# Optimization experiments

Hardware: AMD Instinct MI355X
Metric: run time of the kernel (lower is better)

The kernel has to match this reference:

```python
import jax, jax.numpy as jnp
import numpy as np

OUT_GRID = (256, 256)  # output_grid_shape


def setup_inputs() -> dict:
    key = jax.random.key(0)
    k1, k2 = jax.random.split(key)
    N, H, W, C = 16, 256, 256, 32
    x = jax.random.normal(k1, (N, H, W, C), dtype=jnp.float32)
    # loc network: global mean pool -> dense(6); small weights + identity-affine bias
    W_loc = jax.random.normal(k2, (C, 6), dtype=jnp.float32) * 0.01
    b_loc = jnp.array([1.0, 0.0, 0.0, 0.0, 1.0, 0.0], dtype=jnp.float32)
    return {"x": x, "W_loc": W_loc, "b_loc": b_loc}


def _spatial_transform(x, W_loc, b_loc):
    N, H, W, C = x.shape
    Ho, Wo = OUT_GRID
    # loc_network: params (N, 6) -> theta (N, 2, 3)
    params = jnp.mean(x, axis=(1, 2)) @ W_loc + b_loc
    theta = params.reshape(N, 2, 3)
    # grid_transform_fn: affine on [-1,1]-normalized output index grid
    gy = jnp.linspace(-1.0, 1.0, Ho, dtype=jnp.float32)
    gx = jnp.linspace(-1.0, 1.0, Wo, dtype=jnp.float32)
    Gy, Gx = jnp.meshgrid(gy, gx, indexing="ij")
    grid = jnp.stack([Gy.ravel(), Gx.ravel(), jnp.ones(Ho * Wo, jnp.float32)], axis=0)  # (3, Ho*Wo)
    coords = jnp.einsum("npq,qm->npm", theta, grid).reshape(N, 2, Ho, Wo)  # in ~[-1,1]
    # interpolate_bilinear with clip (wrap=False)
    maxes = jnp.array([H - 1, W - 1], dtype=jnp.float32)
    up = (coords + 1.0) * maxes[None, :, None, None] * 0.5  # upscale to pixel coords
    f = jnp.floor(up)
    frac = up - f  # (N, 2, Ho, Wo)
    fi = f.astype(jnp.int32)
    batch = jnp.arange(N)[:, None, None]
    out = jnp.zeros((N, Ho, Wo, C), dtype=x.dtype)
    for by in (0, 1):  # 2^dim corner offsets (bitfield)
        for bx in (0, 1):
            cy = jnp.clip(fi[:, 0] + by, 0, H - 1)
            cx = jnp.clip(fi[:, 1] + bx, 0, W - 1)
            wy = frac[:, 0] if by else 1.0 - frac[:, 0]
            wx = frac[:, 1] if bx else 1.0 - frac[:, 1]
            out = out + x[batch, cy, cx] * (wy * wx)[..., None]
    return out


def reference(x, W_loc, b_loc):
    return _spatial_transform(x, W_loc, b_loc)
```

## Files before the change

### kernel.cpp

```cpp
#include <hip/hip_runtime.h>


#define NIMG 16
#define HDIM 256
#define WDIM 256
#define CH   32
#define HW   (HDIM * WDIM)
#define BPI  64
#define STAGE_PX 384

typedef float f32x4 __attribute__((ext_vector_type(4)));

__global__ __launch_bounds__(256) void st_sum_kernel(
    const float* __restrict__ x, float* __restrict__ partials) {
    const int n   = blockIdx.x >> 6;
    const int blk = blockIdx.x & (BPI - 1);
    const int tid = threadIdx.x;
    const int cg  = tid & 7;
    const int sp  = tid >> 3;

    const float4* xp = (const float4*)(x + (size_t)n * HW * CH);
    float4 a0 = make_float4(0.f, 0.f, 0.f, 0.f);
    float4 a1 = make_float4(0.f, 0.f, 0.f, 0.f);
    float4 a2 = make_float4(0.f, 0.f, 0.f, 0.f);
    float4 a3 = make_float4(0.f, 0.f, 0.f, 0.f);
    int s = blk * 32 + sp;
    #pragma unroll
    for (int it = 0; it < 8; ++it) {
        float4 v0 = xp[(size_t)(s       ) * 8 + cg];
        float4 v1 = xp[(size_t)(s + 2048) * 8 + cg];
        float4 v2 = xp[(size_t)(s + 4096) * 8 + cg];
        float4 v3 = xp[(size_t)(s + 6144) * 8 + cg];
        a0.x += v0.x; a0.y += v0.y; a0.z += v0.z; a0.w += v0.w;
        a1.x += v1.x; a1.y += v1.y; a1.z += v1.z; a1.w += v1.w;
        a2.x += v2.x; a2.y += v2.y; a2.z += v2.z; a2.w += v2.w;
        a3.x += v3.x; a3.y += v3.y; a3.z += v3.z; a3.w += v3.w;
        s += 8192;
    }
    a0.x += a1.x; a0.y += a1.y; a0.z += a1.z; a0.w += a1.w;
    a2.x += a3.x; a2.y += a3.y; a2.z += a3.z; a2.w += a3.w;
    a0.x += a2.x; a0.y += a2.y; a0.z += a2.z; a0.w += a2.w;

    __shared__ float4 red[256];
    red[tid] = a0;
    __syncthreads();
    for (int stride = 16; stride >= 1; stride >>= 1) {
        if (sp < stride) {
            float4 o = red[(sp + stride) * 8 + cg];
            a0.x += o.x; a0.y += o.y; a0.z += o.z; a0.w += o.w;
            red[tid] = a0;
        }
        __syncthreads();
    }
    if (sp == 0) {
        ((float4*)(partials + ((size_t)blk * NIMG + n) * CH))[cg] = a0;
    }
}

__global__ __launch_bounds__(256) void st_interp_kernel(
    const float* __restrict__ x, const float* __restrict__ partials,
    const float* __restrict__ W_loc, const float* __restrict__ b_loc,
    float* __restrict__ out) {
    const int bid = (int)blockIdx.x;
    const int swz = (bid & 7) * 512 + (bid >> 3);
    const int n   = swz >> 8;
    const int r   = swz & 255;
    const int tid = threadIdx.x;

    __shared__ float  red2[8][CH];
    __shared__ float  th_s[8];
    __shared__ float4 stage[STAGE_PX * 8];

    {
        const int c = tid & 31, g = tid >> 5;
        float s = 0.f;
        #pragma unroll
        for (int j = 0; j < 8; ++j)
            s += partials[(size_t)((g * 8 + j) * NIMG + n) * CH + c];
        red2[g][c] = s;
        __syncthreads();
        if (g == 0) {
            float m = 0.f;
            #pragma unroll
            for (int j = 0; j < 8; ++j) m += red2[j][c];
            red2[0][c] = m * (1.0f / (float)HW);
        }
        __syncthreads();
        if (tid < 6) {
            float acc = b_loc[tid];
            for (int c2 = 0; c2 < CH; ++c2)
                acc = fmaf(red2[0][c2], W_loc[c2 * 6 + tid], acc);
            th_s[tid] = acc;
        }
        __syncthreads();
    }
    const float t00 = th_s[0], t01 = th_s[1], t02 = th_s[2];
    const float t10 = th_s[3], t11 = th_s[4], t12 = th_s[5];

    const int ty = r >> 3, tx = r & 7;
    const int row0 = ty * 8, col0 = tx * 32;
    const int p  = tid >> 3;
    const int cg = tid & 7;
    const int wo = col0 + p;

    const float gx  = fmaf((float)wo, 2.0f / 255.0f, -1.0f);
    const float ayx = fmaf(t01, gx, t02);
    const float axx = fmaf(t11, gx, t12);

    const float gyA = fmaf((float)row0,        2.0f / 255.0f, -1.0f);
    const float gyB = fmaf((float)(row0 + 7),  2.0f / 255.0f, -1.0f);
    const float gxA = fmaf((float)col0,        2.0f / 255.0f, -1.0f);
    const float gxB = fmaf((float)(col0 + 31), 2.0f / 255.0f, -1.0f);
    const float uy1 = (fmaf(t00, gyA, fmaf(t01, gxA, t02)) + 1.0f) * 127.5f;
    const float uy2 = (fmaf(t00, gyA, fmaf(t01, gxB, t02)) + 1.0f) * 127.5f;
    const float uy3 = (fmaf(t00, gyB, fmaf(t01, gxA, t02)) + 1.0f) * 127.5f;
    const float uy4 = (fmaf(t00, gyB, fmaf(t01, gxB, t02)) + 1.0f) * 127.5f;
    const float ux1 = (fmaf(t10, gyA, fmaf(t11, gxA, t12)) + 1.0f) * 127.5f;
    const float ux2 = (fmaf(t10, gyA, fmaf(t11, gxB, t12)) + 1.0f) * 127.5f;
    const float ux3 = (fmaf(t10, gyB, fmaf(t11, gxA, t12)) + 1.0f) * 127.5f;
    const float ux4 = (fmaf(t10, gyB, fmaf(t11, gxB, t12)) + 1.0f) * 127.5f;
    const float uymin = fminf(fminf(uy1, uy2), fminf(uy3, uy4));
    const float uymax = fmaxf(fmaxf(uy1, uy2), fmaxf(uy3, uy4));
    const float uxmin = fminf(fminf(ux1, ux2), fminf(ux3, ux4));
    const float uxmax = fmaxf(fmaxf(ux1, ux2), fmaxf(ux3, ux4));
    const int iy_lo = min(max((int)floorf(uymin),     0), HDIM - 1);
    const int iy_hi = min(max((int)floorf(uymax) + 1, 0), HDIM - 1);
    const int ix_lo = min(max((int)floorf(uxmin),     0), WDIM - 1);
    const int ix_hi = min(max((int)floorf(uxmax) + 1, 0), WDIM - 1);
    const int Rr = iy_hi - iy_lo + 1;
    const int Cc = ix_hi - ix_lo + 1;
    const bool finite = (uymin == uymin) && (uymax == uymax) &&
                        (uxmin == uxmin) && (uxmax == uxmax);
    const bool fits = finite && Rr >= 1 && Cc >= 1 && (Rr * Cc) <= STAGE_PX;

    const float4* xp = (const float4*)(x + (size_t)n * HW * CH);
    f32x4* op = (f32x4*)(out + (size_t)n * HW * CH);

    if (fits) {
        const int C8 = Cc * 8;
        for (int rr = 0; rr < Rr; ++rr) {
            const float4* src = xp + ((size_t)((iy_lo + rr) * WDIM + ix_lo)) * 8;
            float4* dst = stage + rr * C8;
            for (int u = tid; u < C8; u += 256) dst[u] = src[u];
        }
        __syncthreads();

        #pragma unroll
        for (int k = 0; k < 8; ++k) {
            const int ho = row0 + k;
            const float gy = fmaf((float)ho, 2.0f / 255.0f, -1.0f);
            const float uy = (fmaf(t00, gy, ayx) + 1.0f) * 127.5f;
            const float ux = (fmaf(t10, gy, axx) + 1.0f) * 127.5f;
            const float fy = floorf(uy), fx = floorf(ux);
            const float ry = uy - fy, rx = ux - fx;
            const int iy0 = min(max((int)fy,     0), HDIM - 1);
            const int iy1 = min(max((int)fy + 1, 0), HDIM - 1);
            const int ix0 = min(max((int)fx,     0), WDIM - 1);
            const int ix1 = min(max((int)fx + 1, 0), WDIM - 1);
            const int ly0 = iy0 - iy_lo, ly1 = iy1 - iy_lo;
            const int lx0 = ix0 - ix_lo, lx1 = ix1 - ix_lo;
            float4 v00 = stage[(ly0 * Cc + lx0) * 8 + cg];
            float4 v01 = stage[(ly0 * Cc + lx1) * 8 + cg];
            float4 v10 = stage[(ly1 * Cc + lx0) * 8 + cg];
            float4 v11 = stage[(ly1 * Cc + lx1) * 8 + cg];
            const float w00 = (1.0f - ry) * (1.0f - rx);
            const float w01 = (1.0f - ry) * rx;
            const float w10 = ry * (1.0f - rx);
            const float w11 = ry * rx;
            f32x4 o;
            o.x = v00.x * w00 + v01.x * w01 + v10.x * w10 + v11.x * w11;
            o.y = v00.y * w00 + v01.y * w01 + v10.y * w10 + v11.y * w11;
            o.z = v00.z * w00 + v01.z * w01 + v10.z * w10 + v11.z * w11;
            o.w = v00.w * w00 + v01.w * w01 + v10.w * w10 + v11.w * w11;
            __builtin_nontemporal_store(o, &op[(size_t)(ho * WDIM + wo) * 8 + cg]);
        }
    } else {
        for (int k = 0; k < 8; ++k) {
            const int ho = row0 + k;
            const float gy = fmaf((float)ho, 2.0f / 255.0f, -1.0f);
            const float uy = (fmaf(t00, gy, ayx) + 1.0f) * 127.5f;
            const float ux = (fmaf(t10, gy, axx) + 1.0f) * 127.5f;
            const float fy = floorf(uy), fx = floorf(ux);
            const float ry = uy - fy, rx = ux - fx;
            const int iy0 = min(max((int)fy,     0), HDIM - 1);
            const int iy1 = min(max((int)fy + 1, 0), HDIM - 1);
            const int ix0 = min(max((int)fx,     0), WDIM - 1);
            const int ix1 = min(max((int)fx + 1, 0), WDIM - 1);
            float4 v00 = xp[(size_t)(iy0 * WDIM + ix0) * 8 + cg];
            float4 v01 = xp[(size_t)(iy0 * WDIM + ix1) * 8 + cg];
            float4 v10 = xp[(size_t)(iy1 * WDIM + ix0) * 8 + cg];
            float4 v11 = xp[(size_t)(iy1 * WDIM + ix1) * 8 + cg];
            const float w00 = (1.0f - ry) * (1.0f - rx);
            const float w01 = (1.0f - ry) * rx;
            const float w10 = ry * (1.0f - rx);
            const float w11 = ry * rx;
            f32x4 o;
            o.x = v00.x * w00 + v01.x * w01 + v10.x * w10 + v11.x * w11;
            o.y = v00.y * w00 + v01.y * w01 + v10.y * w10 + v11.y * w11;
            o.z = v00.z * w00 + v01.z * w01 + v10.z * w10 + v11.z * w11;
            o.w = v00.w * w00 + v01.w * w01 + v10.w * w10 + v11.w * w11;
            __builtin_nontemporal_store(o, &op[(size_t)(ho * WDIM + wo) * 8 + cg]);
        }
    }
}

extern "C" void kernel_launch(void* const* d_in, const int* in_sizes, int n_in,
                              void* d_out, int out_size, void* d_ws, size_t ws_size,
                              hipStream_t stream) {
    const float* x     = (const float*)d_in[0];
    const float* W_loc = (const float*)d_in[1];
    const float* b_loc = (const float*)d_in[2];
    float* out = (float*)d_out;

    float* partials = (float*)d_ws;

    st_sum_kernel<<<NIMG * BPI, 256, 0, stream>>>(x, partials);
    st_interp_kernel<<<NIMG * (HW / 256), 256, 0, stream>>>(
        x, partials, W_loc, b_loc, out);
}
```

Baseline: 75.60 us.

## Speculatively prefetch fixed halo window into registers before theta computation

The interp kernel now issues the global loads for a fixed 10x36-pixel window around the output tile, with a 1-row and 2-column halo, into registers before it reduces partials and computes theta. The tile loads therefore overlap the loc-network latency instead of waiting on it. The values are written to LDS only if the transformed footprint falls inside this fixed window, which near-identity affines should satisfy; otherwise the existing global-gather fallback runs. This costs 12 float4 registers per thread and a possibly wasted load when the window misses, and a fixed stride removes the dynamic Cc indexing.

```diff
diff --git a/kernel.cpp b/kernel.cpp
--- a/kernel.cpp
+++ b/kernel.cpp
@@ -7,7 +7,12 @@
 #define CH   32
 #define HW   (HDIM * WDIM)
 #define BPI  64
-#define STAGE_PX 384
+
+#define R_CAP 10
+#define C_CAP 36
+#define C8    (C_CAP * 8)
+#define STAGE_N (R_CAP * C8)
+#define NLD   12
 
 typedef float f32x4 __attribute__((ext_vector_type(4)));
 
@@ -67,9 +72,28 @@
     const int r   = swz & 255;
     const int tid = threadIdx.x;
 
+    const int ty = r >> 3, tx = r & 7;
+    const int row0 = ty * 8, col0 = tx * 32;
+
     __shared__ float  red2[8][CH];
     __shared__ float  th_s[8];
-    __shared__ float4 stage[STAGE_PX * 8];
+    __shared__ float4 stage[STAGE_N];
+
+    const float4* xp = (const float4*)(x + (size_t)n * HW * CH);
+
+    float4 buf[NLD];
+    #pragma unroll
+    for (int i = 0; i < NLD; ++i) {
+        const int u = tid + i * 256;
+        if (u < STAGE_N) {
+            const int rr  = u / C8;
+            const int m   = u - rr * C8;
+            const int lx  = m >> 3, c2 = m & 7;
+            const int sy  = min(max(row0 - 1 + rr, 0), HDIM - 1);
+            const int sx  = min(max(col0 - 2 + lx, 0), WDIM - 1);
+            buf[i] = xp[(size_t)(sy * WDIM + sx) * 8 + c2];
+        }
+    }
 
     {
         const int c = tid & 31, g = tid >> 5;
@@ -96,16 +120,6 @@
     }
     const float t00 = th_s[0], t01 = th_s[1], t02 = th_s[2];
     const float t10 = th_s[3], t11 = th_s[4], t12 = th_s[5];
-
-    const int ty = r >> 3, tx = r & 7;
-    const int row0 = ty * 8, col0 = tx * 32;
-    const int p  = tid >> 3;
-    const int cg = tid & 7;
-    const int wo = col0 + p;
-
-    const float gx  = fmaf((float)wo, 2.0f / 255.0f, -1.0f);
-    const float ayx = fmaf(t01, gx, t02);
-    const float axx = fmaf(t11, gx, t12);
 
     const float gyA = fmaf((float)row0,        2.0f / 255.0f, -1.0f);
     const float gyB = fmaf((float)(row0 + 7),  2.0f / 255.0f, -1.0f);
@@ -117,34 +131,33 @@
     const float uy4 = (fmaf(t00, gyB, fmaf(t01, gxB, t02)) + 1.0f) * 127.5f;
     const float ux1 = (fmaf(t10, gyA, fmaf(t11, gxA, t12)) + 1.0f) * 127.5f;
     const float ux2 = (fmaf(t10, gyA, fmaf(t11, gxB, t12)) + 1.0f) * 127.5f;
-    const float ux3 = (fmaf(t10, gyB, fmaf(t11, gxA, t12)) + 1.0f) * 127.5f;
-    const float ux4 = (fmaf(t10, gyB, fmaf(t11, gxB, t12)) + 1.0f) * 127.5f;
+    const float ux3 = (fmaf(t10, gyB, fmaf(t11, gxB, t12)) + 1.0f) * 127.5f;
+    const float ux4 = (fmaf(t10, gyB, fmaf(t11, gxA, t12)) + 1.0f) * 127.5f;
     const float uymin = fminf(fminf(uy1, uy2), fminf(uy3, uy4));
     const float uymax = fmaxf(fmaxf(uy1, uy2), fmaxf(uy3, uy4));
     const float uxmin = fminf(fminf(ux1, ux2), fminf(ux3, ux4));
     const float uxmax = fmaxf(fmaxf(ux1, ux2), fmaxf(ux3, ux4));
-    const int iy_lo = min(max((int)floorf(uymin),     0), HDIM - 1);
-    const int iy_hi = min(max((int)floorf(uymax) + 1, 0), HDIM - 1);
-    const int ix_lo = min(max((int)floorf(uxmin),     0), WDIM - 1);
-    const int ix_hi = min(max((int)floorf(uxmax) + 1, 0), WDIM - 1);
-    const int Rr = iy_hi - iy_lo + 1;
-    const int Cc = ix_hi - ix_lo + 1;
-    const bool finite = (uymin == uymin) && (uymax == uymax) &&
-                        (uxmin == uxmin) && (uxmax == uxmax);
-    const bool fits = finite && Rr >= 1 && Cc >= 1 && (Rr * Cc) <= STAGE_PX;
-
-    const float4* xp = (const float4*)(x + (size_t)n * HW * CH);
+    const bool fits = (uymin > (float)row0 - 0.9f) && (uymax < (float)row0 + 7.9f) &&
+                      (uxmin > (float)col0 - 1.9f) && (uxmax < (float)col0 + 32.9f);
+
+    const int p  = tid >> 3;
+    const int cg = tid & 7;
+    const int wo = col0 + p;
+    const float gx  = fmaf((float)wo, 2.0f / 255.0f, -1.0f);
+    const float ayx = fmaf(t01, gx, t02);
+    const float axx = fmaf(t11, gx, t12);
+
     f32x4* op = (f32x4*)(out + (size_t)n * HW * CH);
 
     if (fits) {
-        const int C8 = Cc * 8;
-        for (int rr = 0; rr < Rr; ++rr) {
-            const float4* src = xp + ((size_t)((iy_lo + rr) * WDIM + ix_lo)) * 8;
-            float4* dst = stage + rr * C8;
-            for (int u = tid; u < C8; u += 256) dst[u] = src[u];
-        }
-        __syncthreads();
-
+        #pragma unroll
+        for (int i = 0; i < NLD; ++i) {
+            const int u = tid + i * 256;
+            if (u < STAGE_N) stage[u] = buf[i];
+        }
+        __syncthreads();
+
+        const int iy_lo = row0 - 1, ix_lo = col0 - 2;
         #pragma unroll
         for (int k = 0; k < 8; ++k) {
             const int ho = row0 + k;
@@ -159,10 +172,10 @@
             const int ix1 = min(max((int)fx + 1, 0), WDIM - 1);
             const int ly0 = iy0 - iy_lo, ly1 = iy1 - iy_lo;
             const int lx0 = ix0 - ix_lo, lx1 = ix1 - ix_lo;
-            float4 v00 = stage[(ly0 * Cc + lx0) * 8 + cg];
-            float4 v01 = stage[(ly0 * Cc + lx1) * 8 + cg];
-            float4 v10 = stage[(ly1 * Cc + lx0) * 8 + cg];
-            float4 v11 = stage[(ly1 * Cc + lx1) * 8 + cg];
+            float4 v00 = stage[(ly0 * C_CAP + lx0) * 8 + cg];
+            float4 v01 = stage[(ly0 * C_CAP + lx1) * 8 + cg];
+            float4 v10 = stage[(ly1 * C_CAP + lx0) * 8 + cg];
+            float4 v11 = stage[(ly1 * C_CAP + lx1) * 8 + cg];
             const float w00 = (1.0f - ry) * (1.0f - rx);
             const float w01 = (1.0f - ry) * rx;
             const float w10 = ry * (1.0f - rx);
```

Result: slower. 116.9 us (+54.6%).
